# Performance work log

Hardware: AMD Instinct MI355X
Metric: run time of the kernel (lower is better)

Reference implementation:

```python
import jax, jax.numpy as jnp
import numpy as np

CF_ITERS = 5
CF_K = 0.02
DECAY = [0.9, 0.93, 0.85, 0.97, 0.88, 0.94]
N_CHAMBERS = 6
RES_DIM = 100
B = 262144

COUPLING = np.array([
    [0.0, -0.3, 0.6, 0.4, -0.2, 0.3],
    [-0.3, 0.0, -0.5, -0.7, 0.6, 0.4],
    [0.6, -0.5, 0.0, 0.3, -0.3, 0.2],
    [0.4, -0.7, 0.3, 0.0, -0.4, 0.5],
    [-0.2, 0.6, -0.3, -0.4, 0.0, 0.3],
    [0.3, 0.4, 0.2, 0.5, 0.3, 0.0]], dtype=np.float32)


def _init_linear(key, c, fan_out, fan_in):
    kw, kb = jax.random.split(key)
    bound = 1.0 / np.sqrt(fan_in)
    W = jax.random.uniform(kw, (c, fan_out, fan_in), jnp.float32, -bound, bound)
    b = jax.random.uniform(kb, (c, fan_out), jnp.float32, -bound, bound)
    return W, b


def setup_inputs() -> dict:
    key = jax.random.key(0)
    ks = jax.random.split(key, 5)
    res = jax.random.normal(ks[0], (B, RES_DIM), jnp.float32)
    W1, b1 = _init_linear(ks[1], N_CHAMBERS, 128, RES_DIM)
    W2, b2 = _init_linear(ks[2], N_CHAMBERS, 64, 128)
    W3, b3 = _init_linear(ks[3], N_CHAMBERS, 32, 64)
    W4, b4 = _init_linear(ks[4], N_CHAMBERS, 1, 32)
    coupling = jnp.asarray(COUPLING)
    return {"res": res, "W1": W1, "b1": b1, "W2": W2, "b2": b2,
            "W3": W3, "b3": b3, "W4": W4, "b4": b4, "coupling": coupling}


def reference(res, W1, b1, W2, b2, W3, b3, W4, b4, coupling):
    silu = jax.nn.silu
    # batched 6 per-chamber MLPs: [B, C, hidden]
    h = silu(jnp.einsum('bd,chd->bch', res, W1) + b1)      # [B,6,128]
    h = silu(jnp.einsum('bch,coh->bco', h, W2) + b2)       # [B,6,64]
    h = silu(jnp.einsum('bco,cpo->bcp', h, W3) + b3)       # [B,6,32]
    raw = (jnp.einsum('bcp,cqp->bcq', h, W4) + b4)[..., 0]  # [B,6]
    act = jax.nn.sigmoid(raw)
    decay = jnp.asarray(DECAY, dtype=jnp.float32)
    for _ in range(CF_ITERS):
        act = act * decay
        # infl[b,i,j] = CF_K * sin(act[b,j] - act[b,i])
        infl = CF_K * jnp.sin(act[:, None, :] - act[:, :, None])  # [B,6,6]
        act = act + jnp.sum(infl * coupling[None], axis=2)
        act = jnp.clip(act, 0.0, 1.0)
    return (act, raw)
```

## Files before the change

### kernel.cpp

```cpp
#include <hip/hip_runtime.h>


typedef unsigned int u32;
typedef __attribute__((ext_vector_type(8))) short bf16x8;
typedef __attribute__((ext_vector_type(4))) float f32x4;

#define RES_DIM 100
#define NCH 6
#define FRAGS_PER_CH 52
#define NFRAG (NCH*FRAGS_PER_CH)
#define WS_BYTES ((size_t)NFRAG*2048)

#define MFMA16 __builtin_amdgcn_mfma_f32_16x16x32_bf16

union FragU { bf16x8 v; u32 u[4]; uint4 q; };

__device__ __forceinline__ void split2(float f0, float f1, u32 &hp, u32 &lp){
    u32 u0 = __float_as_uint(f0), u1 = __float_as_uint(f1);
    u32 h0 = (u0 + 0x7fffu + ((u0>>16)&1u)) & 0xffff0000u;
    u32 h1 = (u1 + 0x7fffu + ((u1>>16)&1u)) & 0xffff0000u;
    hp = (h0 >> 16) | h1;
    float l0 = f0 - __uint_as_float(h0);
    float l1 = f1 - __uint_as_float(h1);
    lp = (__float_as_uint(l0) >> 16) | (__float_as_uint(l1) & 0xffff0000u);
}

__device__ __forceinline__ float silu1(float x){
    return x * __builtin_amdgcn_rcpf(1.f + __expf(-x));
}
__device__ __forceinline__ f32x4 silu4(f32x4 v){
    f32x4 r; r[0]=silu1(v[0]); r[1]=silu1(v[1]); r[2]=silu1(v[2]); r[3]=silu1(v[3]); return r;
}
__device__ __forceinline__ float sin_rev(float x){ return __builtin_amdgcn_sinf(x*0.15915494309189535f); }

__device__ __forceinline__ void load_frag(const u32* __restrict__ wsb, int frag, int lane,
                                          bf16x8 &h, bf16x8 &l){
    const uint4* p = (const uint4*)(wsb + ((size_t)frag << 9) + (lane << 3));
    FragU H, L; H.q = p[0]; L.q = p[1];
    h = H.v; l = L.v;
}

__device__ __forceinline__ f32x4 triple(f32x4 acc, bf16x8 ah, bf16x8 al, bf16x8 bh, bf16x8 bl){
    acc = MFMA16(ah, bh, acc, 0, 0, 0);
    acc = MFMA16(al, bh, acc, 0, 0, 0);
    acc = MFMA16(ah, bl, acc, 0, 0, 0);
    return acc;
}

__global__ void __launch_bounds__(64) prep_kernel(
    const float* __restrict__ W1, const float* __restrict__ W2,
    const float* __restrict__ W3, u32* __restrict__ ws)
{
    const int f = blockIdx.x;
    const int lane = threadIdx.x;
    const int c = f / FRAGS_PER_CH, r = f % FRAGS_PER_CH;
    const int n15 = lane & 15, quad = lane >> 4;
    float vals[8];
    if (r < 32) {
        int n = r >> 2, k = r & 3;
        const float* wp = W1 + (size_t)c*128*RES_DIM + (size_t)(n*16 + n15)*RES_DIM;
        #pragma unroll
        for (int j=0;j<8;j++){
            int kk = k*32 + quad*8 + j;
            vals[j] = (kk < RES_DIM) ? wp[kk] : 0.f;
        }
    } else if (r < 48) {
        int rr = r - 32; int n = rr >> 2, k = rr & 3;
        const float* wp = W2 + (size_t)c*64*128 + (size_t)(n*16 + n15)*128;
        #pragma unroll
        for (int j=0;j<8;j++) vals[j] = wp[k*32 + quad*8 + j];
    } else {
        int rr = r - 48; int n = rr >> 1, k = rr & 1;
        const float* wp = W3 + (size_t)c*32*64 + (size_t)(n*16 + n15)*64;
        #pragma unroll
        for (int j=0;j<8;j++) vals[j] = wp[k*32 + quad*8 + j];
    }
    u32 hp[4], lp[4];
    #pragma unroll
    for (int i=0;i<4;i++) split2(vals[2*i], vals[2*i+1], hp[i], lp[i]);
    u32* dst = ws + ((size_t)f << 9) + (lane << 3);
    *(uint4*)(dst)     = make_uint4(hp[0],hp[1],hp[2],hp[3]);
    *(uint4*)(dst + 4) = make_uint4(lp[0],lp[1],lp[2],lp[3]);
}

#define TB_STRIDE 36
#define TB_SIZE (32*TB_STRIDE)

__global__ void __launch_bounds__(256, 2) chambers_mfma(
    const float* __restrict__ res, const u32* __restrict__ wsb,
    const float* __restrict__ b1, const float* __restrict__ b2,
    const float* __restrict__ b3, const float* __restrict__ W4,
    const float* __restrict__ b4, const float* __restrict__ Cpl,
    float* __restrict__ out, int nsamp)
{
    __shared__ __align__(16) float tb[4][TB_SIZE];
    __shared__ float rawld[4*32*7];

    const int tid  = threadIdx.x;
    const int w    = tid >> 6, lane = tid & 63;
    const int n15  = lane & 15, quad = lane >> 4;
    const int m_base = (blockIdx.x * 4 + w) * 32;

    bf16x8 rh[2][4], rl[2][4];
    #pragma unroll
    for (int mt=0; mt<2; mt++){
        const float* row = res + (size_t)(m_base + mt*16 + n15) * RES_DIM;
        #pragma unroll
        for (int ks=0; ks<4; ks++){
            float v[8];
            if (ks < 3){
                float4 A = *(const float4*)(row + ks*32 + quad*8);
                float4 B = *(const float4*)(row + ks*32 + quad*8 + 4);
                v[0]=A.x; v[1]=A.y; v[2]=A.z; v[3]=A.w;
                v[4]=B.x; v[5]=B.y; v[6]=B.z; v[7]=B.w;
            } else {
                float4 A = make_float4(0.f,0.f,0.f,0.f);
                if (quad == 0) A = *(const float4*)(row + 96);
                v[0]=A.x; v[1]=A.y; v[2]=A.z; v[3]=A.w;
                v[4]=0.f; v[5]=0.f; v[6]=0.f; v[7]=0.f;
            }
            FragU H, L;
            #pragma unroll
            for (int i=0;i<4;i++) split2(v[2*i], v[2*i+1], H.u[i], L.u[i]);
            rh[mt][ks]=H.v; rl[mt][ks]=L.v;
        }
    }

    for (int c=0; c<NCH; c++){
        const float* b1c = b1 + c*128;
        const float* b2c = b2 + c*64;
        const float* b3c = b3 + c*32;
        const int fbase = c*FRAGS_PER_CH;

        f32x4 c2[2][4];
        #pragma unroll
        for (int mt=0; mt<2; mt++)
            #pragma unroll
            for (int nt=0; nt<4; nt++){
                float bb = b2c[nt*16 + n15];
                f32x4 t = {bb,bb,bb,bb}; c2[mt][nt] = t;
            }

        for (int kk=0; kk<4; kk++){
            bf16x8 w2h[4], w2l[4];
            #pragma unroll
            for (int nt=0; nt<4; nt++) load_frag(wsb, fbase + 32 + nt*4 + kk, lane, w2h[nt], w2l[nt]);

            #pragma unroll
            for (int pp=0; pp<2; pp++){
                int p = kk*2 + pp;
                float bb = b1c[p*16 + n15];
                f32x4 z = {0.f,0.f,0.f,0.f};
                f32x4 A0h = {bb,bb,bb,bb}, A0u = z, A0v = z;
                f32x4 A1h = A0h,           A1u = z, A1v = z;
                #pragma unroll
                for (int ks=0; ks<4; ks++){
                    bf16x8 bh, bl; load_frag(wsb, fbase + p*4 + ks, lane, bh, bl);
                    A0h = MFMA16(rh[0][ks], bh, A0h, 0,0,0);
                    A1h = MFMA16(rh[1][ks], bh, A1h, 0,0,0);
                    A0u = MFMA16(rl[0][ks], bh, A0u, 0,0,0);
                    A1u = MFMA16(rl[1][ks], bh, A1u, 0,0,0);
                    A0v = MFMA16(rh[0][ks], bl, A0v, 0,0,0);
                    A1v = MFMA16(rh[1][ks], bl, A1v, 0,0,0);
                }
                f32x4 s0 = silu4((A0h + A0u) + A0v);
                f32x4 s1 = silu4((A1h + A1u) + A1v);
                #pragma unroll
                for (int r=0; r<4; r++){
                    tb[w][(quad*4 + r)*TB_STRIDE      + pp*16 + n15] = s0[r];
                    tb[w][(16 + quad*4 + r)*TB_STRIDE + pp*16 + n15] = s1[r];
                }
            }
            __threadfence_block();
            bf16x8 a2h[2], a2l[2];
            #pragma unroll
            for (int mt=0; mt<2; mt++){
                const float* qp = &tb[w][(mt*16 + n15)*TB_STRIDE + quad*8];
                float4 A = *(const float4*)qp;
                float4 B = *(const float4*)(qp + 4);
                FragU H, L;
                split2(A.x, A.y, H.u[0], L.u[0]);
                split2(A.z, A.w, H.u[1], L.u[1]);
                split2(B.x, B.y, H.u[2], L.u[2]);
                split2(B.z, B.w, H.u[3], L.u[3]);
                a2h[mt]=H.v; a2l[mt]=L.v;
            }
            __threadfence_block();
            #pragma unroll
            for (int nt=0; nt<4; nt++){
                c2[0][nt] = triple(c2[0][nt], a2h[0], a2l[0], w2h[nt], w2l[nt]);
                c2[1][nt] = triple(c2[1][nt], a2h[1], a2l[1], w2h[nt], w2l[nt]);
            }
        }
        #pragma unroll
        for (int mt=0; mt<2; mt++)
            #pragma unroll
            for (int nt=0; nt<4; nt++) c2[mt][nt] = silu4(c2[mt][nt]);

        f32x4 c3[2][2];
        #pragma unroll
        for (int mt=0; mt<2; mt++)
            #pragma unroll
            for (int nt=0; nt<2; nt++){
                float bb = b3c[nt*16 + n15];
                f32x4 t = {bb,bb,bb,bb}; c3[mt][nt] = t;
            }
        for (int k3=0; k3<2; k3++){
            bf16x8 w3h[2], w3l[2];
            #pragma unroll
            for (int nt=0; nt<2; nt++) load_frag(wsb, fbase + 48 + nt*2 + k3, lane, w3h[nt], w3l[nt]);
            #pragma unroll
            for (int mt=0; mt<2; mt++)
                #pragma unroll
                for (int q2=0; q2<2; q2++)
                    #pragma unroll
                    for (int r=0; r<4; r++)
                        tb[w][(mt*16 + quad*4 + r)*TB_STRIDE + q2*16 + n15] = c2[mt][2*k3+q2][r];
            __threadfence_block();
            bf16x8 a3h[2], a3l[2];
            #pragma unroll
            for (int mt=0; mt<2; mt++){
                const float* qp = &tb[w][(mt*16 + n15)*TB_STRIDE + quad*8];
                float4 A = *(const float4*)qp;
                float4 B = *(const float4*)(qp + 4);
                FragU H, L;
                split2(A.x, A.y, H.u[0], L.u[0]);
                split2(A.z, A.w, H.u[1], L.u[1]);
                split2(B.x, B.y, H.u[2], L.u[2]);
                split2(B.z, B.w, H.u[3], L.u[3]);
                a3h[mt]=H.v; a3l[mt]=L.v;
            }
            __threadfence_block();
            #pragma unroll
            for (int nt=0; nt<2; nt++){
                c3[0][nt] = triple(c3[0][nt], a3h[0], a3l[0], w3h[nt], w3l[nt]);
                c3[1][nt] = triple(c3[1][nt], a3h[1], a3l[1], w3h[nt], w3l[nt]);
            }
        }
        #pragma unroll
        for (int mt=0; mt<2; mt++)
            #pragma unroll
            for (int nt=0; nt<2; nt++) c3[mt][nt] = silu4(c3[mt][nt]);

        float w4a = W4[c*32 + n15];
        float w4b = W4[c*32 + 16 + n15];
        float bb4 = b4[c];
        #pragma unroll
        for (int mt=0; mt<2; mt++){
            float t0 = c3[mt][0][0]*w4a + c3[mt][1][0]*w4b;
            float t1 = c3[mt][0][1]*w4a + c3[mt][1][1]*w4b;
            float t2 = c3[mt][0][2]*w4a + c3[mt][1][2]*w4b;
            float t3 = c3[mt][0][3]*w4a + c3[mt][1][3]*w4b;
            #pragma unroll
            for (int off=1; off<16; off<<=1){
                t0 += __shfl_xor(t0, off, 64);
                t1 += __shfl_xor(t1, off, 64);
                t2 += __shfl_xor(t2, off, 64);
                t3 += __shfl_xor(t3, off, 64);
            }
            if (n15 == 0){
                int mb = w*32 + mt*16 + quad*4;
                rawld[(mb+0)*7 + c] = t0 + bb4;
                rawld[(mb+1)*7 + c] = t1 + bb4;
                rawld[(mb+2)*7 + c] = t2 + bb4;
                rawld[(mb+3)*7 + c] = t3 + bb4;
            }
        }
    }
    __threadfence_block();

    const int m = lane & 31;
    float rw[6], a[6];
    #pragma unroll
    for (int j=0;j<6;j++){
        rw[j] = rawld[(w*32 + m)*7 + j];
        a[j]  = __builtin_amdgcn_rcpf(1.f + __expf(-rw[j]));
    }
    const float dec[6] = {0.9f,0.93f,0.85f,0.97f,0.88f,0.94f};
    float C[6][6];
    #pragma unroll
    for (int i=0;i<6;i++)
        #pragma unroll
        for (int j=0;j<6;j++) C[i][j] = Cpl[i*6+j];
    #pragma unroll
    for (int it=0; it<5; it++){
        #pragma unroll
        for (int j=0;j<6;j++) a[j] *= dec[j];
        float nz[6];
        #pragma unroll
        for (int i=0;i<6;i++){
            float sum = 0.f;
            #pragma unroll
            for (int j=0;j<6;j++) sum += sin_rev(a[j]-a[i]) * C[i][j];
            nz[i] = a[i] + 0.02f*sum;
        }
        #pragma unroll
        for (int i=0;i<6;i++) a[i] = fminf(fmaxf(nz[i],0.f),1.f);
    }
    if (lane < 32){
        size_t s = (size_t)m_base + m;
        #pragma unroll
        for (int j=0;j<6;j++) out[s*6 + j] = a[j];
        size_t rb = (size_t)nsamp*6 + s*6;
        #pragma unroll
        for (int j=0;j<6;j++) out[rb + j] = rw[j];
    }
}

__global__ void __launch_bounds__(256, 2) chambers_fb(
    const float* __restrict__ res, const float* __restrict__ W1, const float* __restrict__ b1,
    const float* __restrict__ W2, const float* __restrict__ b2,
    const float* __restrict__ W3, const float* __restrict__ b3,
    const float* __restrict__ W4, const float* __restrict__ b4,
    const float* __restrict__ Cpl, float* __restrict__ out, int nsamp)
{
    __shared__ float w2t[128*64];
    __shared__ float h3buf[256][33];
    __shared__ float rawbuf[256][7];
    const int tid = threadIdx.x;
    const long long s = (long long)blockIdx.x * 256 + tid;
    float rf[RES_DIM];
    {
        const float4* rp = (const float4*)(res + s*RES_DIM);
        #pragma unroll
        for (int i=0;i<25;i++){
            float4 v = rp[i];
            rf[4*i+0]=v.x; rf[4*i+1]=v.y; rf[4*i+2]=v.z; rf[4*i+3]=v.w;
        }
    }
    for (int c=0;c<6;c++){
        __syncthreads();
        {
            const float* w2c = W2 + c*64*128;
            for (int k=tid; k<64*128; k+=256){
                int o = k >> 7, u = k & 127;
                w2t[u*64 + o] = w2c[k];
            }
        }
        __syncthreads();
        const float* w1c = W1 + c*128*RES_DIM;
        const float* b1c = b1 + c*128;
        const float* b2c = b2 + c*64;
        float h2a[64];
        #pragma unroll
        for (int o=0;o<64;o++) h2a[o] = b2c[o];
        for (int u=0; u<128; u+=2){
            const float4* wa = (const float4*)(w1c + u*RES_DIM);
            const float4* wb = wa + 25;
            float a0=0.f,a1=0.f,a2=0.f,a3=0.f;
            #pragma unroll
            for (int i=0;i<25;i++){
                float4 va=wa[i], vb=wb[i];
                a0 = fmaf(va.x, rf[4*i+0], a0); a0 = fmaf(va.y, rf[4*i+1], a0);
                a2 = fmaf(va.z, rf[4*i+2], a2); a2 = fmaf(va.w, rf[4*i+3], a2);
                a1 = fmaf(vb.x, rf[4*i+0], a1); a1 = fmaf(vb.y, rf[4*i+1], a1);
                a3 = fmaf(vb.z, rf[4*i+2], a3); a3 = fmaf(vb.w, rf[4*i+3], a3);
            }
            float hh0 = silu1(a0+a2+b1c[u]);
            float hh1 = silu1(a1+a3+b1c[u+1]);
            const float* wr0 = &w2t[u*64];
            const float* wr1 = &w2t[(u+1)*64];
            #pragma unroll
            for (int o=0;o<64;o+=4){
                float4 va = *(const float4*)(wr0+o);
                float4 vb = *(const float4*)(wr1+o);
                h2a[o+0] = fmaf(va.x, hh0, fmaf(vb.x, hh1, h2a[o+0]));
                h2a[o+1] = fmaf(va.y, hh0, fmaf(vb.y, hh1, h2a[o+1]));
                h2a[o+2] = fmaf(va.z, hh0, fmaf(vb.z, hh1, h2a[o+2]));
                h2a[o+3] = fmaf(va.w, hh0, fmaf(vb.w, hh1, h2a[o+3]));
            }
        }
        #pragma unroll
        for (int o=0;o<64;o++) h2a[o] = silu1(h2a[o]);
        {
            const float* w3c = W3 + c*32*64;
            const float* b3c = b3 + c*32;
            for (int p=0; p<32; p+=2){
                const float4* wa = (const float4*)(w3c + p*64);
                const float4* wb = wa + 16;
                float a0=0.f,a1=0.f,a2=0.f,a3=0.f;
                #pragma unroll
                for (int k=0;k<16;k++){
                    float4 va=wa[k], vb=wb[k];
                    a0 = fmaf(va.x, h2a[4*k+0], a0); a0 = fmaf(va.y, h2a[4*k+1], a0);
                    a2 = fmaf(va.z, h2a[4*k+2], a2); a2 = fmaf(va.w, h2a[4*k+3], a2);
                    a1 = fmaf(vb.x, h2a[4*k+0], a1); a1 = fmaf(vb.y, h2a[4*k+1], a1);
                    a3 = fmaf(vb.z, h2a[4*k+2], a3); a3 = fmaf(vb.w, h2a[4*k+3], a3);
                }
                h3buf[tid][p]   = silu1(a0+a2+b3c[p]);
                h3buf[tid][p+1] = silu1(a1+a3+b3c[p+1]);
            }
        }
        {
            const float4* w4p = (const float4*)(W4 + c*32);
            float a0=0.f, a1=0.f;
            #pragma unroll
            for (int k=0;k<8;k++){
                float4 v = w4p[k];
                a0 = fmaf(v.x, h3buf[tid][4*k+0], a0);
                a1 = fmaf(v.y, h3buf[tid][4*k+1], a1);
                a0 = fmaf(v.z, h3buf[tid][4*k+2], a0);
                a1 = fmaf(v.w, h3buf[tid][4*k+3], a1);
            }
            rawbuf[tid][c] = a0+a1+b4[c];
        }
    }
    float a[6], rw[6];
    #pragma unroll
    for (int j=0;j<6;j++){ rw[j]=rawbuf[tid][j]; a[j]=__builtin_amdgcn_rcpf(1.f+__expf(-rw[j])); }
    const float dec[6] = {0.9f,0.93f,0.85f,0.97f,0.88f,0.94f};
    float C[6][6];
    #pragma unroll
    for (int i=0;i<6;i++)
        #pragma unroll
        for (int j=0;j<6;j++) C[i][j]=Cpl[i*6+j];
    #pragma unroll
    for (int it=0; it<5; it++){
        #pragma unroll
        for (int j=0;j<6;j++) a[j]*=dec[j];
        float nz[6];
        #pragma unroll
        for (int i=0;i<6;i++){
            float sum=0.f;
            #pragma unroll
            for (int j=0;j<6;j++) sum += sin_rev(a[j]-a[i]) * C[i][j];
            nz[i]=a[i]+0.02f*sum;
        }
        #pragma unroll
        for (int i=0;i<6;i++) a[i]=fminf(fmaxf(nz[i],0.f),1.f);
    }
    long long ob = s*6;
    #pragma unroll
    for (int j=0;j<6;j++) out[ob+j] = a[j];
    long long rb = (long long)nsamp*6 + ob;
    #pragma unroll
    for (int j=0;j<6;j++) out[rb+j] = rw[j];
}

extern "C" void kernel_launch(void* const* d_in, const int* in_sizes, int n_in,
                              void* d_out, int out_size, void* d_ws, size_t ws_size,
                              hipStream_t stream) {
    const float* res = (const float*)d_in[0];
    const float* W1  = (const float*)d_in[1];
    const float* b1  = (const float*)d_in[2];
    const float* W2  = (const float*)d_in[3];
    const float* b2  = (const float*)d_in[4];
    const float* W3  = (const float*)d_in[5];
    const float* b3  = (const float*)d_in[6];
    const float* W4  = (const float*)d_in[7];
    const float* b4  = (const float*)d_in[8];
    const float* Cpl = (const float*)d_in[9];
    float* out = (float*)d_out;
    int nsamp = in_sizes[0] / RES_DIM;

    if (ws_size >= WS_BYTES) {
        u32* ws = (u32*)d_ws;
        prep_kernel<<<NFRAG, 64, 0, stream>>>(W1, W2, W3, ws);
        chambers_mfma<<<nsamp/128, 256, 0, stream>>>(res, ws, b1, b2, b3, W4, b4, Cpl, out, nsamp);
    } else {
        chambers_fb<<<nsamp/256, 256, 0, stream>>>(res, W1, b1, W2, b2, W3, b3, W4, b4, Cpl, out, nsamp);
    }
}
```

Before: 444.5 us.

## Cut register pressure to raise occupancy and repack prep kernel blocks

The main kernel's launch bound goes from 2 to 3 waves-per-EU target. Register use is cut by merging the two correction accumulators of layer 1 into one and by loading the W2/W3 weight fragments just before each use instead of preloading arrays of them. The prep kernel now packs four fragments per 256-thread block. The higher occupancy is meant to hide memory and MFMA latency, at the cost of a serial dependency chain on the merged accumulator, later weight loads, and possible spills.

```diff
diff --git a/kernel.cpp b/kernel.cpp
--- a/kernel.cpp
+++ b/kernel.cpp
@@ -33,9 +33,9 @@
 }
 __device__ __forceinline__ float sin_rev(float x){ return __builtin_amdgcn_sinf(x*0.15915494309189535f); }
 
-__device__ __forceinline__ void load_frag(const u32* __restrict__ wsb, int frag, int lane,
+__device__ __forceinline__ void load_frag(const u32* __restrict__ base, int frag, int lane,
                                           bf16x8 &h, bf16x8 &l){
-    const uint4* p = (const uint4*)(wsb + ((size_t)frag << 9) + (lane << 3));
+    const uint4* p = (const uint4*)(base + ((size_t)frag << 9) + (lane << 3));
     FragU H, L; H.q = p[0]; L.q = p[1];
     h = H.v; l = L.v;
 }
@@ -47,12 +47,12 @@
     return acc;
 }
 
-__global__ void __launch_bounds__(64) prep_kernel(
+__global__ void __launch_bounds__(256) prep_kernel(
     const float* __restrict__ W1, const float* __restrict__ W2,
     const float* __restrict__ W3, u32* __restrict__ ws)
 {
-    const int f = blockIdx.x;
-    const int lane = threadIdx.x;
+    const int f = blockIdx.x * 4 + (threadIdx.x >> 6);
+    const int lane = threadIdx.x & 63;
     const int c = f / FRAGS_PER_CH, r = f % FRAGS_PER_CH;
     const int n15 = lane & 15, quad = lane >> 4;
     float vals[8];
@@ -86,7 +86,7 @@
 #define TB_STRIDE 36
 #define TB_SIZE (32*TB_STRIDE)
 
-__global__ void __launch_bounds__(256, 2) chambers_mfma(
+__global__ void __launch_bounds__(256, 3) chambers_mfma(
     const float* __restrict__ res, const u32* __restrict__ wsb,
     const float* __restrict__ b1, const float* __restrict__ b2,
     const float* __restrict__ b3, const float* __restrict__ W4,
@@ -130,7 +130,7 @@
         const float* b1c = b1 + c*128;
         const float* b2c = b2 + c*64;
         const float* b3c = b3 + c*32;
-        const int fbase = c*FRAGS_PER_CH;
+        const u32* wsc = wsb + ((size_t)(c*FRAGS_PER_CH) << 9);
 
         f32x4 c2[2][4];
         #pragma unroll
@@ -142,29 +142,25 @@
             }
 
         for (int kk=0; kk<4; kk++){
-            bf16x8 w2h[4], w2l[4];
-            #pragma unroll
-            for (int nt=0; nt<4; nt++) load_frag(wsb, fbase + 32 + nt*4 + kk, lane, w2h[nt], w2l[nt]);
-
             #pragma unroll
             for (int pp=0; pp<2; pp++){
                 int p = kk*2 + pp;
                 float bb = b1c[p*16 + n15];
                 f32x4 z = {0.f,0.f,0.f,0.f};
-                f32x4 A0h = {bb,bb,bb,bb}, A0u = z, A0v = z;
-                f32x4 A1h = A0h,           A1u = z, A1v = z;
+                f32x4 A0h = {bb,bb,bb,bb}, A0c = z;
+                f32x4 A1h = A0h,           A1c = z;
                 #pragma unroll
                 for (int ks=0; ks<4; ks++){
-                    bf16x8 bh, bl; load_frag(wsb, fbase + p*4 + ks, lane, bh, bl);
+                    bf16x8 bh, bl; load_frag(wsc, p*4 + ks, lane, bh, bl);
                     A0h = MFMA16(rh[0][ks], bh, A0h, 0,0,0);
                     A1h = MFMA16(rh[1][ks], bh, A1h, 0,0,0);
-                    A0u = MFMA16(rl[0][ks], bh, A0u, 0,0,0);
-                    A1u = MFMA16(rl[1][ks], bh, A1u, 0,0,0);
-                    A0v = MFMA16(rh[0][ks], bl, A0v, 0,0,0);
-                    A1v = MFMA16(rh[1][ks], bl, A1v, 0,0,0);
+                    A0c = MFMA16(rl[0][ks], bh, A0c, 0,0,0);
+                    A1c = MFMA16(rl[1][ks], bh, A1c, 0,0,0);
+                    A0c = MFMA16(rh[0][ks], bl, A0c, 0,0,0);
+                    A1c = MFMA16(rh[1][ks], bl, A1c, 0,0,0);
                 }
-                f32x4 s0 = silu4((A0h + A0u) + A0v);
-                f32x4 s1 = silu4((A1h + A1u) + A1v);
+                f32x4 s0 = silu4(A0h + A0c);
+                f32x4 s1 = silu4(A1h + A1c);
                 #pragma unroll
                 for (int r=0; r<4; r++){
                     tb[w][(quad*4 + r)*TB_STRIDE      + pp*16 + n15] = s0[r];
@@ -188,8 +184,9 @@
             __threadfence_block();
             #pragma unroll
             for (int nt=0; nt<4; nt++){
-                c2[0][nt] = triple(c2[0][nt], a2h[0], a2l[0], w2h[nt], w2l[nt]);
-                c2[1][nt] = triple(c2[1][nt], a2h[1], a2l[1], w2h[nt], w2l[nt]);
+                bf16x8 w2h, w2l; load_frag(wsc, 32 + nt*4 + kk, lane, w2h, w2l);
+                c2[0][nt] = triple(c2[0][nt], a2h[0], a2l[0], w2h, w2l);
+                c2[1][nt] = triple(c2[1][nt], a2h[1], a2l[1], w2h, w2l);
             }
         }
         #pragma unroll
@@ -206,9 +203,6 @@
                 f32x4 t = {bb,bb,bb,bb}; c3[mt][nt] = t;
             }
         for (int k3=0; k3<2; k3++){
-            bf16x8 w3h[2], w3l[2];
-            #pragma unroll
-            for (int nt=0; nt<2; nt++) load_frag(wsb, fbase + 48 + nt*2 + k3, lane, w3h[nt], w3l[nt]);
             #pragma unroll
             for (int mt=0; mt<2; mt++)
                 #pragma unroll
@@ -233,8 +227,9 @@
             __threadfence_block();
             #pragma unroll
             for (int nt=0; nt<2; nt++){
-                c3[0][nt] = triple(c3[0][nt], a3h[0], a3l[0], w3h[nt], w3l[nt]);
-                c3[1][nt] = triple(c3[1][nt], a3h[1], a3l[1], w3h[nt], w3l[nt]);
+                bf16x8 w3h, w3l; load_frag(wsc, 48 + nt*2 + k3, lane, w3h, w3l);
+                c3[0][nt] = triple(c3[0][nt], a3h[0], a3l[0], w3h, w3l);
+                c3[1][nt] = triple(c3[1][nt], a3h[1], a3l[1], w3h, w3l);
             }
         }
         #pragma unroll
@@ -455,7 +450,7 @@
 
     if (ws_size >= WS_BYTES) {
         u32* ws = (u32*)d_ws;
-        prep_kernel<<<NFRAG, 64, 0, stream>>>(W1, W2, W3, ws);
+        prep_kernel<<<NFRAG/4, 256, 0, stream>>>(W1, W2, W3, ws);
         chambers_mfma<<<nsamp/128, 256, 0, stream>>>(res, ws, b1, b2, b3, W4, b4, Cpl, out, nsamp);
     } else {
         chambers_fb<<<nsamp/256, 256, 0, stream>>>(res, W1, b1, W2, b2, W3, b3, W4, b4, Cpl, out, nsamp);
```

Result: slower. 513.3 us (+15.5%).
